# Optimization experiments

Measured on AMD Instinct MI355X. Metric: run time of the kernel, lower is better.

The kernel has to match this reference:

```python
import jax, jax.numpy as jnp
import numpy as np

CHANNELS_CHOICE = np.array([8, 16, 24, 32, 40, 48, 56, 64])
MAX_C = 64
B, H, W_SP = 128, 32, 32
N_EDGES = 6
# edge list per intermediate node: (edge_weight_index, source_node_index)
EDGES = [[(0, 0)], [(1, 0), (2, 1)], [(3, 0), (4, 1), (5, 2)]]


def setup_inputs() -> dict:
    key = jax.random.key(0)
    k1, k2, k3, k4 = jax.random.split(key, 4)
    inputs = jax.random.normal(k1, (B, MAX_C, H, W_SP), dtype=jnp.float32)
    alphas1 = jax.random.uniform(k2, (8,), dtype=jnp.float32)  # input-width arch weights
    alphas2 = jax.random.uniform(k3, (8,), dtype=jnp.float32)  # output-width arch weights
    # shared master 3x3 conv weight per edge (OIHW)
    W = jax.random.normal(k4, (N_EDGES, MAX_C, MAX_C, 3, 3), dtype=jnp.float32) * 0.05
    return {"inputs": inputs, "alphas1": alphas1, "alphas2": alphas2, "W": W}


def _channel_scale(alphas1, alphas2, dtype):
    # mask[c, i] = 1 if channel c is inside width choice CHANNELS_CHOICE[i]
    mask = (jnp.arange(MAX_C)[:, None] < jnp.asarray(CHANNELS_CHOICE)[None, :]).astype(dtype)  # [64, 8]
    a_in = mask @ alphas1   # [64] cumulative input-channel weight
    a_out = mask @ alphas2  # [64] cumulative output-channel weight
    return a_out[:, None] * a_in[None, :]  # [64, 64]


def _edge(x, w, scale):
    # weighted-combi of all (c1, c2) channel-sliced sub-convs == one conv with scaled weight
    w_eff = w * scale[:, :, None, None]
    return jax.lax.conv_general_dilated(
        jax.nn.relu(x), w_eff, window_strides=(1, 1), padding="SAME",
        dimension_numbers=("NCHW", "OIHW", "NCHW"))


def reference(inputs, alphas1, alphas2, W):
    scale = _channel_scale(alphas1, alphas2, inputs.dtype)
    nodes = [inputs]
    for node_edges in EDGES:
        feat = 0.0
        for l, src in node_edges:
            feat = feat + _edge(nodes[src], W[l], scale)
        nodes.append(feat)
    return nodes[-1]
```

## Files before the change

### kernel.cpp

```cpp
#include <hip/hip_runtime.h>
#include <hip/hip_bf16.h>


typedef __bf16 bf16x8 __attribute__((ext_vector_type(8)));
typedef float floatx4 __attribute__((ext_vector_type(4)));
typedef unsigned int uint32;

#define PADW 34
#define PIMG (PADW * PADW)
#define ROWB (PADW * 64 * 2)
#define A_LDS (18 * ROWB)
#define A_CHUNKS (A_LDS / 16)
#define TAPB (64 * 64 * 2)
#define B_LDS (9 * TAPB)
#define B_CHUNKS (B_LDS / 16)
#define SMEM_BYTES (A_LDS + B_LDS)

__device__ __forceinline__ void gld16(const char* g, char* l) {
    __builtin_amdgcn_global_load_lds(
        (const __attribute__((address_space(1))) uint32*)g,
        (__attribute__((address_space(3))) uint32*)l, 16, 0, 0);
}

__global__ __launch_bounds__(256) void pre_kernel(
    const float* __restrict__ in, const float* __restrict__ a1,
    const float* __restrict__ a2, const float* __restrict__ W,
    __hip_bfloat16* __restrict__ wt, __hip_bfloat16* __restrict__ r0,
    __hip_bfloat16* __restrict__ r1, __hip_bfloat16* __restrict__ r2) {
    __shared__ float tile[32][65];
    int blk = blockIdx.x;
    int tid = threadIdx.x;

    if (blk < 864) {
        int idx = blk * 256 + tid;
        int i = idx & 63;
        int o = (idx >> 6) & 63;
        int rest = idx >> 12;
        int t = rest % 9;
        int l = rest / 9;
        int ji = i >> 3, jo = o >> 3;
        float ain = 0.f, aout = 0.f;
#pragma unroll
        for (int j = 0; j < 8; ++j) {
            ain  += (j >= ji) ? a1[j] : 0.f;
            aout += (j >= jo) ? a2[j] : 0.f;
        }
        float v = W[(size_t)((l * 64 + o) * 64 + i) * 9 + t] * ain * aout;
        size_t e = (size_t)(l * 9 + t) * 4096 + o * 64 +
                   ((((i >> 3) ^ (o & 7)) << 3) + (i & 7));
        wt[e] = __float2bfloat16(v);
    } else if (blk < 992) {
        int b = blk - 864;
        __hip_bfloat16* bufs[3] = {r0, r1, r2};
#pragma unroll
        for (int f = 0; f < 3; ++f) {
            uint32* buf = (uint32*)(bufs[f] + (size_t)b * PIMG * 64);
            for (int idx = tid; idx < 132 * 32; idx += 256) {
                int slot = idx >> 5, u = idx & 31;
                int yy, xx;
                if (slot < 34)      { yy = 0;  xx = slot; }
                else if (slot < 68) { yy = 33; xx = slot - 34; }
                else { int s2 = slot - 68; yy = 1 + (s2 >> 1); xx = (s2 & 1) * 33; }
                buf[(size_t)(yy * PADW + xx) * 32 + u] = 0u;
            }
        }
    } else {
        int rb = blk - 992;
        int b = rb >> 5, y = rb & 31;
        int x = tid & 31, c0 = tid >> 5;
        const float* ip = in + ((size_t)b * 64 * 32 + y) * 32 + x;
#pragma unroll
        for (int cc = 0; cc < 8; ++cc) {
            int c = cc * 8 + c0;
            tile[x][c] = fmaxf(ip[(size_t)c * 1024], 0.f);
        }
        __syncthreads();
        int o = tid & 63, xg = tid >> 6;
        int p0 = (b * PADW + y + 1) * PADW + 1;
#pragma unroll
        for (int xx = 0; xx < 8; ++xx) {
            int xq = xx * 4 + xg;
            int p = p0 + xq;
            size_t e = (size_t)p * 64 + ((((o >> 3) ^ (p & 7)) << 3) + (o & 7));
            r0[e] = __float2bfloat16(tile[xq][o]);
        }
    }
}

template <int NSRC, bool FINAL>
__global__ __launch_bounds__(512, 2) void conv_stage(
    const __hip_bfloat16* __restrict__ s0,
    const __hip_bfloat16* __restrict__ s1,
    const __hip_bfloat16* __restrict__ s2,
    const __hip_bfloat16* __restrict__ wt,
    void* __restrict__ dstv, int l0) {
    extern __shared__ char smem[];
    char* smemB = smem + A_LDS;
    int tid = threadIdx.x;
    int wv = tid >> 6, lane = tid & 63;
    int quad = lane >> 4, l15 = lane & 15;
    int blk = blockIdx.x;
    int b = blk >> 1, y0 = (blk & 1) << 4;

    const char* srcs[3] = {(const char*)s0, (const char*)s1, (const char*)s2};
    const char* gW = (const char*)wt + (size_t)l0 * 9 * (size_t)TAPB;

    auto stage_A = [&](int s) {
        const char* gA = srcs[s] + (size_t)(b * PADW + y0) * PADW * 128;
#pragma unroll
        for (int it = 0; it < 10; ++it) {
            int c = it * 512 + tid;
            if (it < 9 || tid < A_CHUNKS - 9 * 512)
                gld16(gA + (size_t)c * 16, smem + (it * 512 + wv * 64) * 16);
        }
    };
    auto stage_B = [&](int s) {
        const char* gB = gW + (size_t)s * 9 * TAPB;
#pragma unroll
        for (int it = 0; it < 9; ++it) {
            int c = it * 512 + tid;
            gld16(gB + (size_t)c * 16, smemB + (it * 512 + wv * 64) * 16);
        }
    };

    floatx4 acc[4][4];
#pragma unroll
    for (int m = 0; m < 4; ++m)
#pragma unroll
        for (int n = 0; n < 4; ++n) acc[m][n] = (floatx4){0.f, 0.f, 0.f, 0.f};

    stage_A(0);
    stage_B(0);
    __syncthreads();

#pragma unroll 1
    for (int s = 0; s < NSRC; ++s) {
#pragma unroll
        for (int tl = 0; tl < 9; ++tl) {
            const int ky = tl / 3, kx = tl % 3;
#pragma unroll
            for (int q = 0; q < 2; ++q) {
                bf16x8 Af[4], Bf[4];
#pragma unroll
                for (int m = 0; m < 4; ++m) {
                    int arow = 2 * wv + (m >> 1) + ky;
                    int apx  = ((m & 1) << 4) + l15 + kx;
                    int R = b * PADW + y0 + arow;
                    int slot = ((q << 2) + quad) ^ ((2 * R + apx) & 7);
                    Af[m] = *(const bf16x8*)(smem + arow * ROWB +
                                             apx * 128 + slot * 16);
                }
#pragma unroll
                for (int n = 0; n < 4; ++n) {
                    int o = (n << 4) + l15;
                    int slot = ((q << 2) + quad) ^ (l15 & 7);
                    Bf[n] = *(const bf16x8*)(smemB + tl * TAPB +
                                             o * 128 + slot * 16);
                }
#pragma unroll
                for (int m = 0; m < 4; ++m)
#pragma unroll
                    for (int n = 0; n < 4; ++n)
                        acc[m][n] = __builtin_amdgcn_mfma_f32_16x16x32_bf16(
                            Af[m], Bf[n], acc[m][n], 0, 0, 0);
            }
        }
        if (s + 1 < NSRC) {
            __syncthreads();
            stage_A(s + 1);
            stage_B(s + 1);
            __syncthreads();
        }
    }

    if (FINAL) {
        float* out = (float*)dstv;
#pragma unroll
        for (int m = 0; m < 4; ++m) {
            int row = y0 + 2 * wv + (m >> 1);
#pragma unroll
            for (int n = 0; n < 4; ++n) {
                int o = (n << 4) + l15;
                *(floatx4*)(out + (((size_t)b * 64 + o) * 32 + row) * 32 +
                            ((m & 1) << 4) + (quad << 2)) = acc[m][n];
            }
        }
    } else {
        __hip_bfloat16* out = (__hip_bfloat16*)dstv;
#pragma unroll
        for (int m = 0; m < 4; ++m) {
            int row = y0 + 2 * wv + (m >> 1);
#pragma unroll
            for (int n = 0; n < 4; ++n) {
                int o = (n << 4) + l15;
#pragma unroll
                for (int r = 0; r < 4; ++r) {
                    int x = ((m & 1) << 4) + (quad << 2) + r;
                    int p = (b * PADW + row + 1) * PADW + x + 1;
                    float v = fmaxf(acc[m][n][r], 0.f);
                    size_t e = (size_t)p * 64 +
                               ((((o >> 3) ^ (p & 7)) << 3) + (o & 7));
                    out[e] = __float2bfloat16(v);
                }
            }
        }
    }
}

extern "C" void kernel_launch(void* const* d_in, const int* in_sizes, int n_in,
                              void* d_out, int out_size, void* d_ws,
                              size_t ws_size, hipStream_t stream) {
    const float* inputs  = (const float*)d_in[0];
    const float* alphas1 = (const float*)d_in[1];
    const float* alphas2 = (const float*)d_in[2];
    const float* W       = (const float*)d_in[3];
    char* ws = (char*)d_ws;

    __hip_bfloat16* wt = (__hip_bfloat16*)(ws);
    __hip_bfloat16* r0 = (__hip_bfloat16*)(ws + ((size_t)1 << 20));
    __hip_bfloat16* r1 = (__hip_bfloat16*)(ws + ((size_t)20 << 20));
    __hip_bfloat16* r2 = (__hip_bfloat16*)(ws + ((size_t)40 << 20));
    float* out = (float*)d_out;

    (void)hipFuncSetAttribute((const void*)conv_stage<1, false>,
                              hipFuncAttributeMaxDynamicSharedMemorySize,
                              SMEM_BYTES);
    (void)hipFuncSetAttribute((const void*)conv_stage<2, false>,
                              hipFuncAttributeMaxDynamicSharedMemorySize,
                              SMEM_BYTES);
    (void)hipFuncSetAttribute((const void*)conv_stage<3, true>,
                              hipFuncAttributeMaxDynamicSharedMemorySize,
                              SMEM_BYTES);

    pre_kernel<<<864 + 128 + 4096, 256, 0, stream>>>(inputs, alphas1, alphas2,
                                                     W, wt, r0, r1, r2);
    conv_stage<1, false><<<256, 512, SMEM_BYTES, stream>>>(r0, r1, r2, wt,
                                                           (void*)r1, 0);
    conv_stage<2, false><<<256, 512, SMEM_BYTES, stream>>>(r0, r1, r2, wt,
                                                           (void*)r2, 1);
    conv_stage<3, true ><<<256, 512, SMEM_BYTES, stream>>>(r0, r1, r2, wt,
                                                           (void*)out, 3);
}
```

Before: 151.0 us.

## Fuse preprocessing and three conv stages into one cooperative kernel with grid syncs

Merges the preprocessing kernel and the three conv stage kernels into a single persistent cooperative kernel of 256 blocks, separated by grid-wide barriers, to remove launch gaps and tail effects between the four launches. The preprocessing work is redistributed over 256 blocks of 512 threads. The MFMA inner loop also double-buffers its LDS fragment loads so the next half-tap is read while the current one computes. If the cooperative launch fails, it falls back to separate launches. The risks are grid-sync overhead, higher register pressure from the doubled fragments, and a slower pre phase on fewer blocks.

```diff
diff --git a/kernel.cpp b/kernel.cpp
--- a/kernel.cpp
+++ b/kernel.cpp
@@ -1,5 +1,8 @@
 #include <hip/hip_runtime.h>
 #include <hip/hip_bf16.h>
+#include <hip/hip_cooperative_groups.h>
+
+namespace cg = cooperative_groups;
 
 
 typedef __bf16 bf16x8 __attribute__((ext_vector_type(8)));
@@ -13,7 +16,6 @@
 #define A_CHUNKS (A_LDS / 16)
 #define TAPB (64 * 64 * 2)
 #define B_LDS (9 * TAPB)
-#define B_CHUNKS (B_LDS / 16)
 #define SMEM_BYTES (A_LDS + B_LDS)
 
 __device__ __forceinline__ void gld16(const char* g, char* l) {
@@ -22,22 +24,17 @@
         (__attribute__((address_space(3))) uint32*)l, 16, 0, 0);
 }
 
-__global__ __launch_bounds__(256) void pre_kernel(
+__device__ __forceinline__ void pre_phase(
+    int blk, int tid, char* smem,
     const float* __restrict__ in, const float* __restrict__ a1,
     const float* __restrict__ a2, const float* __restrict__ W,
     __hip_bfloat16* __restrict__ wt, __hip_bfloat16* __restrict__ r0,
     __hip_bfloat16* __restrict__ r1, __hip_bfloat16* __restrict__ r2) {
-    __shared__ float tile[32][65];
-    int blk = blockIdx.x;
-    int tid = threadIdx.x;
-
-    if (blk < 864) {
-        int idx = blk * 256 + tid;
-        int i = idx & 63;
-        int o = (idx >> 6) & 63;
+    for (int t = tid; t < 864; t += 512) {
+        int idx = blk * 864 + t;
+        int i = idx & 63, o = (idx >> 6) & 63;
         int rest = idx >> 12;
-        int t = rest % 9;
-        int l = rest / 9;
+        int tt = rest % 9, l = rest / 9;
         int ji = i >> 3, jo = o >> 3;
         float ain = 0.f, aout = 0.f;
 #pragma unroll
@@ -45,17 +42,17 @@
             ain  += (j >= ji) ? a1[j] : 0.f;
             aout += (j >= jo) ? a2[j] : 0.f;
         }
-        float v = W[(size_t)((l * 64 + o) * 64 + i) * 9 + t] * ain * aout;
-        size_t e = (size_t)(l * 9 + t) * 4096 + o * 64 +
+        float v = W[(size_t)((l * 64 + o) * 64 + i) * 9 + tt] * ain * aout;
+        size_t e = (size_t)(l * 9 + tt) * 4096 + o * 64 +
                    ((((i >> 3) ^ (o & 7)) << 3) + (i & 7));
         wt[e] = __float2bfloat16(v);
-    } else if (blk < 992) {
-        int b = blk - 864;
+    }
+    if (blk < 128) {
         __hip_bfloat16* bufs[3] = {r0, r1, r2};
 #pragma unroll
         for (int f = 0; f < 3; ++f) {
-            uint32* buf = (uint32*)(bufs[f] + (size_t)b * PIMG * 64);
-            for (int idx = tid; idx < 132 * 32; idx += 256) {
+            uint32* buf = (uint32*)(bufs[f] + (size_t)blk * PIMG * 64);
+            for (int idx = tid; idx < 132 * 32; idx += 512) {
                 int slot = idx >> 5, u = idx & 31;
                 int yy, xx;
                 if (slot < 34)      { yy = 0;  xx = slot; }
@@ -64,22 +61,25 @@
                 buf[(size_t)(yy * PADW + xx) * 32 + u] = 0u;
             }
         }
-    } else {
-        int rb = blk - 992;
-        int b = rb >> 5, y = rb & 31;
+    }
+    float (*tile)[65] = (float (*)[65])smem;
+    for (int j = 0; j < 16; ++j) {
+        int rb = (blk << 4) + j;
+        int bb = rb >> 5, y = rb & 31;
+        __syncthreads();
         int x = tid & 31, c0 = tid >> 5;
-        const float* ip = in + ((size_t)b * 64 * 32 + y) * 32 + x;
-#pragma unroll
-        for (int cc = 0; cc < 8; ++cc) {
-            int c = cc * 8 + c0;
+        const float* ip = in + ((size_t)bb * 2048 + y) * 32 + x;
+#pragma unroll
+        for (int cc = 0; cc < 4; ++cc) {
+            int c = (cc << 4) + c0;
             tile[x][c] = fmaxf(ip[(size_t)c * 1024], 0.f);
         }
         __syncthreads();
         int o = tid & 63, xg = tid >> 6;
-        int p0 = (b * PADW + y + 1) * PADW + 1;
-#pragma unroll
-        for (int xx = 0; xx < 8; ++xx) {
-            int xq = xx * 4 + xg;
+        int p0 = (bb * PADW + y + 1) * PADW + 1;
+#pragma unroll
+        for (int xx = 0; xx < 4; ++xx) {
+            int xq = (xx << 3) + xg;
             int p = p0 + xq;
             size_t e = (size_t)p * 64 + ((((o >> 3) ^ (p & 7)) << 3) + (o & 7));
             r0[e] = __float2bfloat16(tile[xq][o]);
@@ -88,22 +88,13 @@
 }
 
 template <int NSRC, bool FINAL>
-__global__ __launch_bounds__(512, 2) void conv_stage(
-    const __hip_bfloat16* __restrict__ s0,
-    const __hip_bfloat16* __restrict__ s1,
-    const __hip_bfloat16* __restrict__ s2,
-    const __hip_bfloat16* __restrict__ wt,
-    void* __restrict__ dstv, int l0) {
-    extern __shared__ char smem[];
+__device__ __forceinline__ void conv_phase(
+    char* smem, const char* s0, const char* s1, const char* s2,
+    const char* wtc, void* dstv, int l0,
+    int b, int y0, int wv, int quad, int l15, int tid) {
     char* smemB = smem + A_LDS;
-    int tid = threadIdx.x;
-    int wv = tid >> 6, lane = tid & 63;
-    int quad = lane >> 4, l15 = lane & 15;
-    int blk = blockIdx.x;
-    int b = blk >> 1, y0 = (blk & 1) << 4;
-
-    const char* srcs[3] = {(const char*)s0, (const char*)s1, (const char*)s2};
-    const char* gW = (const char*)wt + (size_t)l0 * 9 * (size_t)TAPB;
+    const char* srcs[3] = {s0, s1, s2};
+    const char* gW = wtc + (size_t)l0 * 9 * (size_t)TAPB;
 
     auto stage_A = [&](int s) {
         const char* gA = srcs[s] + (size_t)(b * PADW + y0) * PADW * 128;
@@ -135,35 +126,37 @@
 
 #pragma unroll 1
     for (int s = 0; s < NSRC; ++s) {
-#pragma unroll
-        for (int tl = 0; tl < 9; ++tl) {
-            const int ky = tl / 3, kx = tl % 3;
-#pragma unroll
-            for (int q = 0; q < 2; ++q) {
-                bf16x8 Af[4], Bf[4];
-#pragma unroll
-                for (int m = 0; m < 4; ++m) {
-                    int arow = 2 * wv + (m >> 1) + ky;
-                    int apx  = ((m & 1) << 4) + l15 + kx;
-                    int R = b * PADW + y0 + arow;
-                    int slot = ((q << 2) + quad) ^ ((2 * R + apx) & 7);
-                    Af[m] = *(const bf16x8*)(smem + arow * ROWB +
-                                             apx * 128 + slot * 16);
-                }
-#pragma unroll
-                for (int n = 0; n < 4; ++n) {
-                    int o = (n << 4) + l15;
-                    int slot = ((q << 2) + quad) ^ (l15 & 7);
-                    Bf[n] = *(const bf16x8*)(smemB + tl * TAPB +
-                                             o * 128 + slot * 16);
-                }
-#pragma unroll
-                for (int m = 0; m < 4; ++m)
-#pragma unroll
-                    for (int n = 0; n < 4; ++n)
-                        acc[m][n] = __builtin_amdgcn_mfma_f32_16x16x32_bf16(
-                            Af[m], Bf[n], acc[m][n], 0, 0, 0);
-            }
+        bf16x8 Af[2][4], Bf[2][4];
+        auto load_half = [&](int h, int set) {
+            int tl = h >> 1, q = h & 1, ky = tl / 3, kx = tl % 3;
+#pragma unroll
+            for (int m = 0; m < 4; ++m) {
+                int arow = 2 * wv + (m >> 1) + ky;
+                int apx  = ((m & 1) << 4) + l15 + kx;
+                int ph   = (2 * (b * PADW + y0 + arow) + apx) & 7;
+                int slot = ((q << 2) + quad) ^ ph;
+                Af[set][m] = *(const bf16x8*)(smem + arow * ROWB +
+                                              apx * 128 + slot * 16);
+            }
+#pragma unroll
+            for (int n = 0; n < 4; ++n) {
+                int o = (n << 4) + l15;
+                int slot = ((q << 2) + quad) ^ (l15 & 7);
+                Bf[set][n] = *(const bf16x8*)(smemB + tl * TAPB +
+                                              o * 128 + slot * 16);
+            }
+        };
+        load_half(0, 0);
+#pragma unroll
+        for (int h = 0; h < 18; ++h) {
+            if (h + 1 < 18) load_half(h + 1, (h + 1) & 1);
+            const int set = h & 1;
+#pragma unroll
+            for (int m = 0; m < 4; ++m)
+#pragma unroll
+                for (int n = 0; n < 4; ++n)
+                    acc[m][n] = __builtin_amdgcn_mfma_f32_16x16x32_bf16(
+                        Af[set][m], Bf[set][n], acc[m][n], 0, 0, 0);
         }
         if (s + 1 < NSRC) {
             __syncthreads();
@@ -207,6 +200,54 @@
     }
 }
 
+__global__ __launch_bounds__(512, 2) void fused_kernel(
+    const float* __restrict__ in, const float* __restrict__ a1,
+    const float* __restrict__ a2, const float* __restrict__ W,
+    __hip_bfloat16* wt, __hip_bfloat16* r0, __hip_bfloat16* r1,
+    __hip_bfloat16* r2, float* out) {
+    extern __shared__ char smem[];
+    int blk = blockIdx.x, tid = threadIdx.x;
+    pre_phase(blk, tid, smem, in, a1, a2, W, wt, r0, r1, r2);
+    cg::this_grid().sync();
+    int lane = tid & 63;
+    int wv = tid >> 6, quad = lane >> 4, l15 = lane & 15;
+    int b = blk >> 1, y0 = (blk & 1) << 4;
+    conv_phase<1, false>(smem, (const char*)r0, (const char*)r1,
+                         (const char*)r2, (const char*)wt, (void*)r1, 0,
+                         b, y0, wv, quad, l15, tid);
+    cg::this_grid().sync();
+    conv_phase<2, false>(smem, (const char*)r0, (const char*)r1,
+                         (const char*)r2, (const char*)wt, (void*)r2, 1,
+                         b, y0, wv, quad, l15, tid);
+    cg::this_grid().sync();
+    conv_phase<3, true>(smem, (const char*)r0, (const char*)r1,
+                        (const char*)r2, (const char*)wt, (void*)out, 3,
+                        b, y0, wv, quad, l15, tid);
+}
+
+__global__ __launch_bounds__(512) void pre_kernel_sa(
+    const float* __restrict__ in, const float* __restrict__ a1,
+    const float* __restrict__ a2, const float* __restrict__ W,
+    __hip_bfloat16* wt, __hip_bfloat16* r0, __hip_bfloat16* r1,
+    __hip_bfloat16* r2) {
+    extern __shared__ char smem[];
+    pre_phase(blockIdx.x, threadIdx.x, smem, in, a1, a2, W, wt, r0, r1, r2);
+}
+
+template <int NSRC, bool FINAL>
+__global__ __launch_bounds__(512, 2) void conv_sa(
+    const __hip_bfloat16* s0, const __hip_bfloat16* s1,
+    const __hip_bfloat16* s2, const __hip_bfloat16* wt, void* dstv, int l0) {
+    extern __shared__ char smem[];
+    int blk = blockIdx.x, tid = threadIdx.x;
+    int lane = tid & 63;
+    int wv = tid >> 6, quad = lane >> 4, l15 = lane & 15;
+    int b = blk >> 1, y0 = (blk & 1) << 4;
+    conv_phase<NSRC, FINAL>(smem, (const char*)s0, (const char*)s1,
+                            (const char*)s2, (const char*)wt, dstv, l0,
+                            b, y0, wv, quad, l15, tid);
+}
+
 extern "C" void kernel_launch(void* const* d_in, const int* in_sizes, int n_in,
                               void* d_out, int out_size, void* d_ws,
                               size_t ws_size, hipStream_t stream) {
@@ -222,22 +263,38 @@
     __hip_bfloat16* r2 = (__hip_bfloat16*)(ws + ((size_t)40 << 20));
     float* out = (float*)d_out;
 
-    (void)hipFuncSetAttribute((const void*)conv_stage<1, false>,
-                              hipFuncAttributeMaxDynamicSharedMemorySize,
-                              SMEM_BYTES);
-    (void)hipFuncSetAttribute((const void*)conv_stage<2, false>,
-                              hipFuncAttributeMaxDynamicSharedMemorySize,
-                              SMEM_BYTES);
-    (void)hipFuncSetAttribute((const void*)conv_stage<3, true>,
-                              hipFuncAttributeMaxDynamicSharedMemorySize,
-                              SMEM_BYTES);
-
-    pre_kernel<<<864 + 128 + 4096, 256, 0, stream>>>(inputs, alphas1, alphas2,
-                                                     W, wt, r0, r1, r2);
-    conv_stage<1, false><<<256, 512, SMEM_BYTES, stream>>>(r0, r1, r2, wt,
-                                                           (void*)r1, 0);
-    conv_stage<2, false><<<256, 512, SMEM_BYTES, stream>>>(r0, r1, r2, wt,
-                                                           (void*)r2, 1);
-    conv_stage<3, true ><<<256, 512, SMEM_BYTES, stream>>>(r0, r1, r2, wt,
-                                                           (void*)out, 3);
-}
+    (void)hipFuncSetAttribute((const void*)fused_kernel,
+                              hipFuncAttributeMaxDynamicSharedMemorySize,
+                              SMEM_BYTES);
+    (void)hipFuncSetAttribute((const void*)pre_kernel_sa,
+                              hipFuncAttributeMaxDynamicSharedMemorySize,
+                              SMEM_BYTES);
+    (void)hipFuncSetAttribute((const void*)conv_sa<1, false>,
+                              hipFuncAttributeMaxDynamicSharedMemorySize,
+                              SMEM_BYTES);
+    (void)hipFuncSetAttribute((const void*)conv_sa<2, false>,
+                              hipFuncAttributeMaxDynamicSharedMemorySize,
+                              SMEM_BYTES);
+    (void)hipFuncSetAttribute((const void*)conv_sa<3, true>,
+                              hipFuncAttributeMaxDynamicSharedMemorySize,
+                              SMEM_BYTES);
+
+    void* args[9] = {(void*)&inputs, (void*)&alphas1, (void*)&alphas2,
+                     (void*)&W, (void*)&wt, (void*)&r0, (void*)&r1,
+                     (void*)&r2, (void*)&out};
+    hipError_t e = hipLaunchCooperativeKernel((const void*)fused_kernel,
+                                              dim3(256), dim3(512), args,
+                                              (unsigned)SMEM_BYTES, stream);
+    if (e != hipSuccess) {
+        (void)hipGetLastError();
+        pre_kernel_sa<<<256, 512, SMEM_BYTES, stream>>>(inputs, alphas1,
+                                                        alphas2, W, wt, r0,
+                                                        r1, r2);
+        conv_sa<1, false><<<256, 512, SMEM_BYTES, stream>>>(r0, r1, r2, wt,
+                                                            (void*)r1, 0);
+        conv_sa<2, false><<<256, 512, SMEM_BYTES, stream>>>(r0, r1, r2, wt,
+                                                            (void*)r2, 1);
+        conv_sa<3, true ><<<256, 512, SMEM_BYTES, stream>>>(r0, r1, r2, wt,
+                                                            (void*)out, 3);
+    }
+}
```

Measured after the change: 354.1 us. 2.34x slower.
